# Kernel optimization log

Hardware: AMD Instinct MI355X
Metric: run time of the kernel (lower is better)

The kernel has to match this reference:

```python
import jax, jax.numpy as jnp
import numpy as np

B, N, DIM, H = 4, 16384, 384, 8
C = DIM // H          # head_dim = 48
M = C // 2            # kernel_ratio=0.5 -> m = 24
EPS = 1e-6

def setup_inputs() -> dict:
    key = jax.random.key(0)
    k0, k1, k2, k3, k4 = jax.random.split(key, 5)
    x = jax.random.normal(k0, (B, N, DIM), jnp.float32)
    # small init scale keeps exp() in the kernel feature map well-conditioned
    qkv_w = jax.random.normal(k1, (3 * DIM, DIM), jnp.float32) * 0.02
    proj_w = jax.random.normal(k2, (DIM, DIM), jnp.float32) * 0.02
    proj_b = jax.random.normal(k3, (DIM,), jnp.float32) * 0.02
    # per-head orthogonal random features (rows orthonormal), scaled by sqrt(m)
    g = jax.random.normal(k4, (H, C, M), jnp.float32)
    q_mat, _ = jnp.linalg.qr(g)                  # (H, C, M), orthonormal columns
    w = jnp.transpose(q_mat, (0, 2, 1)) * np.sqrt(M)  # (H, M, C)
    return {"x": x, "qkv_w": qkv_w, "proj_w": proj_w, "proj_b": proj_b, "w": w}

def _feature_map(t, w, scale):
    # t: [B,H,N,C], w: [H,M,C]
    t = t * scale
    logits = jnp.einsum('bhnc,hmc->bhnm', t, w) - 0.5 * jnp.sum(t * t, axis=-1, keepdims=True)
    return jnp.exp(logits) / np.sqrt(w.shape[1])

def reference(x, qkv_w, proj_w, proj_b, w):
    b, n, dim = x.shape
    h, m, c = w.shape
    scale = c ** (-0.25)
    # qkv projection, split into q,k,v with layout (qkv H C)
    qkv = (x @ qkv_w.T).reshape(b, n, 3, h, c).transpose(2, 0, 3, 1, 4)  # [3,B,H,N,C]
    q, k, v = qkv[0], qkv[1], qkv[2]
    phi_q = _feature_map(q, w, scale)   # [B,H,N,M]
    phi_k = _feature_map(k, w, scale)   # [B,H,N,M]
    # normalizer: q . sum_n(k)
    D = jnp.einsum('bhnm,bhm->bhn', phi_q, phi_k.sum(axis=2)) + EPS  # [B,H,N]
    # linear-attention state: K^T V, then Q @ (K^T V)
    ktv = jnp.einsum('bhnm,bhnc->bhmc', phi_k, v)                    # [B,H,M,C]
    out = jnp.einsum('bhnm,bhmc->bhnc', phi_q, ktv) / D[..., None]   # [B,H,N,C]
    out = out.transpose(0, 2, 1, 3).reshape(b, n, dim)               # [B,N,dim]
    return out @ proj_w.T + proj_b
```

## Files before the change

kernel.cpp:

```cpp
#include <hip/hip_runtime.h>
#include <hip/hip_bf16.h>

typedef __bf16 bf16x8 __attribute__((ext_vector_type(8)));
typedef float  f32x4  __attribute__((ext_vector_type(4)));
typedef short  short8 __attribute__((ext_vector_type(8)));
typedef float  f32x4v __attribute__((ext_vector_type(4)));

#define B_SZ 4
#define N_SZ 16384
#define DIM_SZ 384
#define H_SZ 8
#define C_SZ 48
#define M_SZ 24

static constexpr float SCALE = 0.37991784282579627f;
static constexpr float RSM   = 0.20412414523193154f;
static constexpr float EPS_V = 1e-6f;


__device__ __forceinline__ void gld_lds16(void* lds, const void* g) {
  __builtin_amdgcn_global_load_lds(
      (const __attribute__((address_space(1))) unsigned int*)g,
      (__attribute__((address_space(3))) unsigned int*)lds, 16, 0, 0);
}

__device__ __forceinline__ float bf2f(short s) {
  union { unsigned u; float f; } cv;
  cv.u = ((unsigned)(unsigned short)s) << 16;
  return cv.f;
}
__device__ __forceinline__ short f2bf_s(float f) {
  const __bf16 b = (__bf16)f;
  return __builtin_bit_cast(short, b);
}

template<int EPI>
__global__ __launch_bounds__(256, 2) void gemm2b(
    const __bf16* __restrict__ A, const __bf16* __restrict__ Bm,
    void* __restrict__ Cout, const float* __restrict__ bias,
    int M, int Nw, int K,
    size_t aSlice, size_t bSlice, size_t cSlice) {
  extern __shared__ __align__(16) char lds[];
  const int t    = threadIdx.x;
  const int lane = t & 63;
  const int wid  = t >> 6;
  const int wm   = wid >> 1;
  const int wn   = wid & 1;
  const int l15  = lane & 15;
  const int kgq  = lane >> 4;

  const int bz = blockIdx.z;
  const __bf16* Ab = A  + (size_t)bz * aSlice;
  const __bf16* Bb = Bm + (size_t)bz * bSlice;

  const int gx   = gridDim.x;
  const int nwg  = gx * gridDim.y;
  const int orig = blockIdx.y * gx + blockIdx.x;
  const int qq   = nwg >> 3, rr = nwg & 7;
  const int xcd  = orig & 7, pos = orig >> 3;
  const int id   = (xcd < rr ? xcd*(qq+1) : rr*(qq+1) + (xcd-rr)*qq) + pos;
  const int row0 = (id / gx) * 128, col0 = (id % gx) * 128;

  const int nt = K >> 6;

  const int sg = (t & 7) ^ ((t >> 3) & 7);

  auto stage = [&](int kt) {
    char* buf = lds + (kt & 1) * 32768;
    const size_t kofs = (size_t)kt * 64 + sg * 8;
    #pragma unroll
    for (int i = 0; i < 4; ++i) {
      const int r = i*32 + (t >> 3);
      gld_lds16(buf + i*4096 + t*16,         Ab + (size_t)(row0 + r) * K + kofs);
      gld_lds16(buf + 16384 + i*4096 + t*16, Bb + (size_t)(col0 + r) * K + kofs);
    }
  };

  f32x4 acc[4][4] = {};

  stage(0);

  for (int kt = 0; kt < nt; ++kt) {
    asm volatile("s_waitcnt vmcnt(0)" ::: "memory");
    __builtin_amdgcn_s_barrier();
    __builtin_amdgcn_sched_barrier(0);

    char* buf = lds + (kt & 1) * 32768;
    if (kt + 1 < nt) stage(kt + 1);

    bf16x8 bfr[4][2];
    #pragma unroll
    for (int ni = 0; ni < 4; ++ni) {
      const int brow = wn*64 + ni*16 + l15;
      #pragma unroll
      for (int kk = 0; kk < 2; ++kk)
        bfr[ni][kk] = *(const bf16x8*)(buf + 16384 + brow*128
                          + ((kk*64 + kgq*16) ^ ((brow & 7) << 4)));
    }
    #pragma unroll
    for (int mi = 0; mi < 4; ++mi) {
      const int arow = wm*64 + mi*16 + l15;
      const bf16x8 a0 = *(const bf16x8*)(buf + arow*128
                          + ((kgq*16)      ^ ((arow & 7) << 4)));
      const bf16x8 a1 = *(const bf16x8*)(buf + arow*128
                          + ((64 + kgq*16) ^ ((arow & 7) << 4)));
      __builtin_amdgcn_s_setprio(1);
      #pragma unroll
      for (int ni = 0; ni < 4; ++ni) {
        acc[mi][ni] = __builtin_amdgcn_mfma_f32_16x16x32_bf16(a0, bfr[ni][0], acc[mi][ni], 0,0,0);
        acc[mi][ni] = __builtin_amdgcn_mfma_f32_16x16x32_bf16(a1, bfr[ni][1], acc[mi][ni], 0,0,0);
      }
      __builtin_amdgcn_s_setprio(0);
    }
  }

  const int cr = (lane >> 4) << 2;
  #pragma unroll
  for (int mi = 0; mi < 4; ++mi) {
    #pragma unroll
    for (int ni = 0; ni < 4; ++ni) {
      const int col = col0 + wn*64 + ni*16 + l15;
      #pragma unroll
      for (int j = 0; j < 4; ++j) {
        const int row = row0 + wm*64 + mi*16 + cr + j;
        const float v = acc[mi][ni][j];
        if (EPI == 1) {
          ((float*)Cout + (size_t)bz*cSlice)[(size_t)row * Nw + col] = v + bias[col];
        } else {
          ((__bf16*)Cout + (size_t)bz*cSlice)[(size_t)row * Nw + col] = (__bf16)v;
        }
      }
    }
  }
}

__global__ __launch_bounds__(256) void wlog_kernel(
    const float* __restrict__ qkv_w, const float* __restrict__ w,
    __bf16* __restrict__ Baug) {
  const int idx = blockIdx.x * 256 + threadIdx.x;
  if (idx >= 2*192*384) return;
  const int d = idx % 384, rs = idx / 384;
  const int side = rs / 192, hm = rs % 192;
  const int h = hm / 24;
  const float* wr = w + (size_t)hm * 48;
  const float* qw = qkv_w + ((size_t)(side*384 + h*48)) * 384 + d;
  float acc = 0.f;
  #pragma unroll
  for (int c = 0; c < 48; ++c)
    acc += wr[c] * qw[(size_t)c * 384];
  Baug[(size_t)(768 + side*192 + hm) * 384 + d] = (__bf16)(acc * SCALE);
}

__global__ __launch_bounds__(256) void ktv_fused(
    const __bf16* __restrict__ kvll, float* __restrict__ ktv_f,
    float* __restrict__ ksum) {
  const int b = blockIdx.z, h = blockIdx.y, sp = blockIdx.x;
  const int t = threadIdx.x, wv = t >> 6, lane = t & 63;
  const int l15 = lane & 15, g = lane >> 4;
  const int bh = b*H_SZ + h;
  __shared__ __align__(16) __bf16 vT[4][48][40];
  __shared__ __align__(16) __bf16 phiT[4][24][40];
  __shared__ float red[4][1152];
  f32x4 acc[2][3] = {};
  f32x4 aks[2] = {};
  const int nbase = sp*512 + wv*128;

  bf16x8 ones{};
  if (l15 == 0)
    #pragma unroll
    for (int j = 0; j < 8; ++j) ones[j] = (__bf16)1.0f;

  for (int step = 0; step < 4; ++step) {
    const int n0 = nbase + step*32;
    #pragma unroll
    for (int it = 0; it < 3; ++it) {
      const int task = it*64 + lane;
      const int tk = task / 6, p = task % 6;
      const short8 r = *(const short8*)(kvll + ((size_t)(b*N_SZ) + n0 + tk)*1152
                                            + 384 + h*C_SZ + p*8);
      #pragma unroll
      for (int e = 0; e < 8; ++e)
        vT[wv][p*8 + e][tk] = __builtin_bit_cast(__bf16, (short)r[e]);
    }
    if (lane < 32) {
      const __bf16* row = kvll + ((size_t)(b*N_SZ) + n0 + lane)*1152 + h*C_SZ;
      float ss = 0.f;
      #pragma unroll
      for (int i = 0; i < 6; ++i) {
        const short8 r = *(const short8*)(row + i*8);
        #pragma unroll
        for (int j = 0; j < 8; ++j) { const float f = bf2f(r[j]) * SCALE; ss += f*f; }
      }
      const float hs = 0.5f * ss;
      const __bf16* lk = kvll + ((size_t)(b*N_SZ) + n0 + lane)*1152 + 960 + h*24;
      #pragma unroll
      for (int i = 0; i < 3; ++i) {
        const short8 r = *(const short8*)(lk + i*8);
        #pragma unroll
        for (int j = 0; j < 8; ++j)
          phiT[wv][i*8 + j][lane] = (__bf16)(__expf(bf2f(r[j]) - hs) * RSM);
      }
    }
    const bf16x8 a0 = *(const bf16x8*)(&phiT[wv][l15][g*8]);
    bf16x8 a1{};
    if (l15 < 8) a1 = *(const bf16x8*)(&phiT[wv][16 + l15][g*8]);
    #pragma unroll
    for (int ct = 0; ct < 3; ++ct) {
      const bf16x8 bfr = *(const bf16x8*)(&vT[wv][ct*16 + l15][g*8]);
      acc[0][ct] = __builtin_amdgcn_mfma_f32_16x16x32_bf16(a0, bfr, acc[0][ct], 0,0,0);
      acc[1][ct] = __builtin_amdgcn_mfma_f32_16x16x32_bf16(a1, bfr, acc[1][ct], 0,0,0);
    }
    aks[0] = __builtin_amdgcn_mfma_f32_16x16x32_bf16(a0, ones, aks[0], 0,0,0);
    aks[1] = __builtin_amdgcn_mfma_f32_16x16x32_bf16(a1, ones, aks[1], 0,0,0);
  }

  if (l15 == 0) {
    #pragma unroll
    for (int mt = 0; mt < 2; ++mt)
      #pragma unroll
      for (int jj = 0; jj < 4; ++jj) {
        const int m = mt*16 + g*4 + jj;
        if (m < 24) atomicAdd(&ksum[bh*24 + m], aks[mt][jj]);
      }
  }
  #pragma unroll
  for (int mt = 0; mt < 2; ++mt)
    #pragma unroll
    for (int ct = 0; ct < 3; ++ct)
      #pragma unroll
      for (int jj = 0; jj < 4; ++jj) {
        const int row = mt*16 + g*4 + jj;
        if (row < 24)
          red[wv][row*48 + ct*16 + l15] = acc[mt][ct][jj];
      }
  __syncthreads();
  for (int i = t; i < 1152; i += 256) {
    const float s = red[0][i] + red[1][i] + red[2][i] + red[3][i];
    atomicAdd(&ktv_f[bh*1152 + i], s);
  }
}

__global__ __launch_bounds__(256) void gt_kernel(
    const float* __restrict__ ktv_f, const float* __restrict__ proj_w,
    __bf16* __restrict__ Gt) {
  const int idx = blockIdx.x * 256 + threadIdx.x;
  if (idx >= 4*384*192) return;
  const int hm = idx % 192, o = (idx / 192) % 384, b = idx / (192*384);
  const int h = hm / 24, m = hm % 24;
  const float* kt = ktv_f + ((size_t)(b*H_SZ + h))*1152 + m*48;
  const float* pw = proj_w + (size_t)o*384 + h*48;
  float acc = 0.f;
  #pragma unroll
  for (int c = 0; c < 48; ++c) acc += kt[c] * pw[c];
  Gt[((size_t)b*384 + o)*192 + hm] = (__bf16)acc;
}

__global__ __launch_bounds__(256) void pprime_kernel(
    const __bf16* __restrict__ kvll, const float* __restrict__ ksum,
    __bf16* __restrict__ Pp) {
  const int tok = blockIdx.x * 256 + threadIdx.x;
  const int b = (blockIdx.x * 256) >> 14;
  __shared__ float ksl[192];
  if (threadIdx.x < 192) ksl[threadIdx.x] = ksum[b*192 + threadIdx.x];
  __syncthreads();

  const __bf16* lq = kvll + (size_t)tok*1152 + 768;
  __bf16* po = Pp + (size_t)tok*192;
  #pragma unroll
  for (int h = 0; h < 8; ++h) {
    float ph[24];
    float d = EPS_V;
    #pragma unroll
    for (int i = 0; i < 3; ++i) {
      const short8 r = *(const short8*)(lq + h*24 + i*8);
      #pragma unroll
      for (int j = 0; j < 8; ++j) {
        const float p = __expf(bf2f(r[j])) * RSM;
        ph[i*8 + j] = p;
        d += p * ksl[h*24 + i*8 + j];
      }
    }
    const float inv = 1.0f / d;
    #pragma unroll
    for (int i = 0; i < 3; ++i) {
      short8 pk;
      #pragma unroll
      for (int j = 0; j < 8; ++j) pk[j] = f2bf_s(ph[i*8 + j] * inv);
      *(short8*)(po + h*24 + i*8) = pk;
    }
  }
}

__global__ __launch_bounds__(256) void f32_to_bf16_kernel(
    const float* __restrict__ in, __bf16* __restrict__ out, int n8) {
  const int i = blockIdx.x * blockDim.x + threadIdx.x;
  if (i >= n8) return;
  const f32x4v a = *(const f32x4v*)(in + (size_t)i*8);
  const f32x4v c = *(const f32x4v*)(in + (size_t)i*8 + 4);
  short8 pk;
  #pragma unroll
  for (int j = 0; j < 4; ++j) {
    pk[j]     = f2bf_s(a[j]);
    pk[4 + j] = f2bf_s(c[j]);
  }
  *(short8*)(out + (size_t)i*8) = pk;
}

extern "C" void kernel_launch(void* const* d_in, const int* in_sizes, int n_in,
                              void* d_out, int out_size, void* d_ws, size_t ws_size,
                              hipStream_t stream) {
  (void)in_sizes; (void)n_in; (void)out_size; (void)ws_size;
  const float* x      = (const float*)d_in[0];
  const float* qkv_w  = (const float*)d_in[1];
  const float* proj_w = (const float*)d_in[2];
  const float* proj_b = (const float*)d_in[3];
  const float* w      = (const float*)d_in[4];
  float* out = (float*)d_out;

  const size_t BN_TOT = (size_t)B_SZ * N_SZ;
  char* ws = (char*)d_ws;
  size_t off = 0;
  auto alloc = [&](size_t bytes) {
    char* p = ws + off;
    off += (bytes + 255) & ~(size_t)255;
    return p;
  };
  __bf16* x_bf  = (__bf16*)alloc(BN_TOT * DIM_SZ * 2);
  __bf16* Baug  = (__bf16*)alloc((size_t)1152 * 384 * 2);
  __bf16* kvll  = (__bf16*)alloc(BN_TOT * 1152 * 2);
  float*  ktv_f = (float*)alloc((size_t)32 * 1152 * 4);
  float*  ksum  = (float*)alloc((size_t)32 * 24 * 4);
  __bf16* Pp    = (__bf16*)alloc(BN_TOT * 192 * 2);
  __bf16* Gt    = (__bf16*)alloc((size_t)B_SZ * 384 * 192 * 2);

  hipMemsetAsync(ktv_f, 0, (size_t)32 * 1152 * 4, stream);
  hipMemsetAsync(ksum,  0, (size_t)32 * 24 * 4, stream);

  static const int LDS_BYTES = 2 * 32768;
  hipFuncSetAttribute(reinterpret_cast<const void*>(&gemm2b<0>),
                      hipFuncAttributeMaxDynamicSharedMemorySize, LDS_BYTES);
  hipFuncSetAttribute(reinterpret_cast<const void*>(&gemm2b<1>),
                      hipFuncAttributeMaxDynamicSharedMemorySize, LDS_BYTES);

  {
    const int n8x = (int)(BN_TOT * DIM_SZ / 8);
    f32_to_bf16_kernel<<<(n8x + 255)/256, 256, 0, stream>>>(x, x_bf, n8x);
    const int n8kv = 768 * 384 / 8;
    f32_to_bf16_kernel<<<(n8kv + 255)/256, 256, 0, stream>>>(
        qkv_w + (size_t)384 * 384, Baug, n8kv);
    wlog_kernel<<<(2*192*384 + 255)/256, 256, 0, stream>>>(qkv_w, w, Baug);
  }

  gemm2b<0><<<dim3(1152/128, BN_TOT/128, 1), 256, LDS_BYTES, stream>>>(
      x_bf, Baug, kvll, nullptr, (int)BN_TOT, 1152, DIM_SZ, 0, 0, 0);

  ktv_fused<<<dim3(32, H_SZ, B_SZ), 256, 0, stream>>>(kvll, ktv_f, ksum);

  gt_kernel<<<(4*384*192 + 255)/256, 256, 0, stream>>>(ktv_f, proj_w, Gt);
  pprime_kernel<<<(int)(BN_TOT/256), 256, 0, stream>>>(kvll, ksum, Pp);

  gemm2b<1><<<dim3(384/128, N_SZ/128, B_SZ), 256, LDS_BYTES, stream>>>(
      Pp, Gt, out, proj_b, N_SZ, 384, 192,
      (size_t)N_SZ * 192, (size_t)384 * 192, (size_t)N_SZ * 384);
}
```

Before: 229.3 us.

## Replace QKV GEMM with 256x256-tile 8-wave ping-pong pipelined kernel

```diff
diff --git a/kernel.cpp b/kernel.cpp
--- a/kernel.cpp
+++ b/kernel.cpp
@@ -32,6 +32,149 @@
 __device__ __forceinline__ short f2bf_s(float f) {
   const __bf16 b = (__bf16)f;
   return __builtin_bit_cast(short, b);
+}
+__device__ __forceinline__ f32x4 MF(bf16x8 a, bf16x8 b, f32x4 c) {
+  return __builtin_amdgcn_mfma_f32_16x16x32_bf16(a, b, c, 0, 0, 0);
+}
+__device__ __forceinline__ void bar_lgkm() {
+  __builtin_amdgcn_s_barrier();
+  asm volatile("s_waitcnt lgkmcnt(0)" ::: "memory");
+  __builtin_amdgcn_sched_barrier(0);
+}
+__device__ __forceinline__ void bar2() {
+  __builtin_amdgcn_s_barrier();
+  __builtin_amdgcn_sched_barrier(0);
+}
+__device__ __forceinline__ void mfmaq(f32x4 (&ac)[4][2],
+                                      const bf16x8 (&a)[4][2],
+                                      const bf16x8 (&b)[2][2]) {
+  __builtin_amdgcn_s_setprio(1);
+  #pragma unroll
+  for (int mf = 0; mf < 4; ++mf) {
+    ac[mf][0] = MF(a[mf][0], b[0][0], ac[mf][0]);
+    ac[mf][0] = MF(a[mf][1], b[0][1], ac[mf][0]);
+    ac[mf][1] = MF(a[mf][0], b[1][0], ac[mf][1]);
+    ac[mf][1] = MF(a[mf][1], b[1][1], ac[mf][1]);
+  }
+  __builtin_amdgcn_s_setprio(0);
+}
+
+__global__ __launch_bounds__(512, 2) void gemm8p(
+    const __bf16* __restrict__ A, const __bf16* __restrict__ Bm,
+    __bf16* __restrict__ Cout, int Nw, int K) {
+  extern __shared__ __align__(16) char lds[];
+  const int t    = threadIdx.x;
+  const int lane = t & 63;
+  const int wid  = t >> 6;
+  const int wm   = wid >> 2;
+  const int wn   = wid & 3;
+  const int l15  = lane & 15;
+  const int kgq  = lane >> 4;
+
+  const int gx   = gridDim.x;
+  const int nwg  = gx * gridDim.y;
+  const int orig = blockIdx.y * gx + blockIdx.x;
+  const int qq   = nwg >> 3, rr = nwg & 7;
+  const int xcd  = orig & 7, pos = orig >> 3;
+  const int id   = (xcd < rr ? xcd*(qq+1) : rr*(qq+1) + (xcd-rr)*qq) + pos;
+  const int row0 = (id / gx) * 256, col0 = (id % gx) * 256;
+
+  const int nt = K >> 6;
+  const int sg = (t & 7) ^ ((t >> 3) & 7);
+
+  auto stageh = [&](int k, int isB, int half) {
+    if (k >= nt) return;
+    char* base = lds + (k & 1) * 65536 + isB * 32768;
+    const __bf16* src = isB ? (Bm + (size_t)col0 * K) : (A + (size_t)row0 * K);
+    #pragma unroll
+    for (int i = 0; i < 2; ++i) {
+      const int r = half*128 + i*64 + (t >> 3);
+      gld_lds16(base + r*128 + (t & 7)*16,
+                src + (size_t)r * K + (size_t)k*64 + sg*8);
+    }
+  };
+  auto loadA = [&](const char* buf, int qm, bf16x8 (&af)[4][2]) {
+    #pragma unroll
+    for (int mf = 0; mf < 4; ++mf) {
+      const int r = qm*128 + wm*64 + mf*16 + l15;
+      af[mf][0] = *(const bf16x8*)(buf + r*128 + ((kgq*16)      ^ ((r&7)<<4)));
+      af[mf][1] = *(const bf16x8*)(buf + r*128 + ((64 + kgq*16) ^ ((r&7)<<4)));
+    }
+  };
+  auto loadB = [&](const char* buf, int qn, bf16x8 (&bq)[2][2]) {
+    #pragma unroll
+    for (int nf = 0; nf < 2; ++nf) {
+      const int r = qn*128 + wn*32 + nf*16 + l15;
+      bq[nf][0] = *(const bf16x8*)(buf + 32768 + r*128 + ((kgq*16)      ^ ((r&7)<<4)));
+      bq[nf][1] = *(const bf16x8*)(buf + 32768 + r*128 + ((64 + kgq*16) ^ ((r&7)<<4)));
+    }
+  };
+
+  f32x4 acc[2][2][4][2] = {};
+  bf16x8 af[4][2], bq0[2][2], bq1[2][2];
+
+  stageh(0, 0, 0); stageh(0, 1, 0); stageh(0, 0, 1); stageh(0, 1, 1);
+  stageh(1, 0, 0); stageh(1, 1, 0);
+  asm volatile("s_waitcnt vmcnt(4)" ::: "memory");
+  __builtin_amdgcn_s_barrier();
+  __builtin_amdgcn_sched_barrier(0);
+
+  const int nIter = nt >> 1;
+  for (int it = 0; it < nIter; ++it) {
+    const int kt1 = 2*it + 1, kt2 = 2*it + 2, kt3 = 2*it + 3;
+    char* b0 = lds;
+    char* b1 = lds + 65536;
+    const bool lastIt = (it == nIter - 1);
+
+    loadA(b0, 0, af); loadB(b0, 0, bq0);
+    stageh(kt1, 0, 1);
+    bar_lgkm(); mfmaq(acc[0][0], af, bq0); bar2();
+    loadB(b0, 1, bq1);
+    stageh(kt1, 1, 1);
+    bar_lgkm(); mfmaq(acc[0][1], af, bq1); bar2();
+    loadA(b0, 1, af);
+    stageh(kt2, 0, 0);
+    bar_lgkm(); mfmaq(acc[1][0], af, bq0); bar2();
+    stageh(kt2, 1, 0);
+    if (lastIt) asm volatile("s_waitcnt vmcnt(0)" ::: "memory");
+    else        asm volatile("s_waitcnt vmcnt(4)" ::: "memory");
+    __builtin_amdgcn_s_barrier();
+    __builtin_amdgcn_sched_barrier(0);
+    mfmaq(acc[1][1], af, bq1); bar2();
+    loadA(b1, 0, af); loadB(b1, 0, bq0);
+    stageh(kt2, 0, 1);
+    bar_lgkm(); mfmaq(acc[0][0], af, bq0); bar2();
+    loadB(b1, 1, bq1);
+    stageh(kt2, 1, 1);
+    bar_lgkm(); mfmaq(acc[0][1], af, bq1); bar2();
+    loadA(b1, 1, af);
+    stageh(kt3, 0, 0);
+    bar_lgkm(); mfmaq(acc[1][0], af, bq0); bar2();
+    stageh(kt3, 1, 0);
+    if (!lastIt) asm volatile("s_waitcnt vmcnt(4)" ::: "memory");
+    __builtin_amdgcn_s_barrier();
+    __builtin_amdgcn_sched_barrier(0);
+    mfmaq(acc[1][1], af, bq1); bar2();
+  }
+
+  const int cr = (lane >> 4) << 2;
+  #pragma unroll
+  for (int qm = 0; qm < 2; ++qm)
+    #pragma unroll
+    for (int qn = 0; qn < 2; ++qn)
+      #pragma unroll
+      for (int mf = 0; mf < 4; ++mf)
+        #pragma unroll
+        for (int nf = 0; nf < 2; ++nf) {
+          const int col = col0 + qn*128 + wn*32 + nf*16 + l15;
+          if (col < Nw) {
+            #pragma unroll
+            for (int j = 0; j < 4; ++j) {
+              const int row = row0 + qm*128 + wm*64 + mf*16 + cr + j;
+              Cout[(size_t)row * Nw + col] = (__bf16)acc[qm][qn][mf][nf][j];
+            }
+          }
+        }
 }
 
 template<int EPI>
@@ -62,7 +205,6 @@
   const int row0 = (id / gx) * 128, col0 = (id % gx) * 128;
 
   const int nt = K >> 6;
-
   const int sg = (t & 7) ^ ((t >> 3) & 7);
 
   auto stage = [&](int kt) {
@@ -77,7 +219,6 @@
   };
 
   f32x4 acc[4][4] = {};
-
   stage(0);
 
   for (int kt = 0; kt < nt; ++kt) {
@@ -107,8 +248,8 @@
       __builtin_amdgcn_s_setprio(1);
       #pragma unroll
       for (int ni = 0; ni < 4; ++ni) {
-        acc[mi][ni] = __builtin_amdgcn_mfma_f32_16x16x32_bf16(a0, bfr[ni][0], acc[mi][ni], 0,0,0);
-        acc[mi][ni] = __builtin_amdgcn_mfma_f32_16x16x32_bf16(a1, bfr[ni][1], acc[mi][ni], 0,0,0);
+        acc[mi][ni] = MF(a0, bfr[ni][0], acc[mi][ni]);
+        acc[mi][ni] = MF(a1, bfr[ni][1], acc[mi][ni]);
       }
       __builtin_amdgcn_s_setprio(0);
     }
@@ -207,11 +348,11 @@
     #pragma unroll
     for (int ct = 0; ct < 3; ++ct) {
       const bf16x8 bfr = *(const bf16x8*)(&vT[wv][ct*16 + l15][g*8]);
-      acc[0][ct] = __builtin_amdgcn_mfma_f32_16x16x32_bf16(a0, bfr, acc[0][ct], 0,0,0);
-      acc[1][ct] = __builtin_amdgcn_mfma_f32_16x16x32_bf16(a1, bfr, acc[1][ct], 0,0,0);
-    }
-    aks[0] = __builtin_amdgcn_mfma_f32_16x16x32_bf16(a0, ones, aks[0], 0,0,0);
-    aks[1] = __builtin_amdgcn_mfma_f32_16x16x32_bf16(a1, ones, aks[1], 0,0,0);
+      acc[0][ct] = MF(a0, bfr, acc[0][ct]);
+      acc[1][ct] = MF(a1, bfr, acc[1][ct]);
+    }
+    aks[0] = MF(a0, ones, aks[0]);
+    aks[1] = MF(a1, ones, aks[1]);
   }
 
   if (l15 == 0) {
@@ -326,7 +467,7 @@
     return p;
   };
   __bf16* x_bf  = (__bf16*)alloc(BN_TOT * DIM_SZ * 2);
-  __bf16* Baug  = (__bf16*)alloc((size_t)1152 * 384 * 2);
+  __bf16* Baug  = (__bf16*)alloc((size_t)1280 * 384 * 2);
   __bf16* kvll  = (__bf16*)alloc(BN_TOT * 1152 * 2);
   float*  ktv_f = (float*)alloc((size_t)32 * 1152 * 4);
   float*  ksum  = (float*)alloc((size_t)32 * 24 * 4);
@@ -336,11 +477,12 @@
   hipMemsetAsync(ktv_f, 0, (size_t)32 * 1152 * 4, stream);
   hipMemsetAsync(ksum,  0, (size_t)32 * 24 * 4, stream);
 
-  static const int LDS_BYTES = 2 * 32768;
-  hipFuncSetAttribute(reinterpret_cast<const void*>(&gemm2b<0>),
-                      hipFuncAttributeMaxDynamicSharedMemorySize, LDS_BYTES);
+  static const int LDS8P = 2 * 65536;
+  static const int LDS2B = 2 * 32768;
+  hipFuncSetAttribute(reinterpret_cast<const void*>(&gemm8p),
+                      hipFuncAttributeMaxDynamicSharedMemorySize, LDS8P);
   hipFuncSetAttribute(reinterpret_cast<const void*>(&gemm2b<1>),
-                      hipFuncAttributeMaxDynamicSharedMemorySize, LDS_BYTES);
+                      hipFuncAttributeMaxDynamicSharedMemorySize, LDS2B);
 
   {
     const int n8x = (int)(BN_TOT * DIM_SZ / 8);
@@ -351,15 +493,15 @@
     wlog_kernel<<<(2*192*384 + 255)/256, 256, 0, stream>>>(qkv_w, w, Baug);
   }
 
-  gemm2b<0><<<dim3(1152/128, BN_TOT/128, 1), 256, LDS_BYTES, stream>>>(
-      x_bf, Baug, kvll, nullptr, (int)BN_TOT, 1152, DIM_SZ, 0, 0, 0);
+  gemm8p<<<dim3(1280/256, BN_TOT/256), 512, LDS8P, stream>>>(
+      x_bf, Baug, kvll, 1152, DIM_SZ);
 
   ktv_fused<<<dim3(32, H_SZ, B_SZ), 256, 0, stream>>>(kvll, ktv_f, ksum);
 
   gt_kernel<<<(4*384*192 + 255)/256, 256, 0, stream>>>(ktv_f, proj_w, Gt);
   pprime_kernel<<<(int)(BN_TOT/256), 256, 0, stream>>>(kvll, ksum, Pp);
 
-  gemm2b<1><<<dim3(384/128, N_SZ/128, B_SZ), 256, LDS_BYTES, stream>>>(
+  gemm2b<1><<<dim3(384/128, N_SZ/128, B_SZ), 256, LDS2B, stream>>>(
       Pp, Gt, out, proj_b, N_SZ, 384, 192,
       (size_t)N_SZ * 192, (size_t)384 * 192, (size_t)N_SZ * 384);
 }
```

After: 255.5 us. 1.11x slower.

## Add single-buffered BK=128 QKV GEMM and double ktv_fused grid split

Applied to the files above, without the earlier changes.

```diff
diff --git a/kernel.cpp b/kernel.cpp
--- a/kernel.cpp
+++ b/kernel.cpp
@@ -32,6 +32,105 @@
 __device__ __forceinline__ short f2bf_s(float f) {
   const __bf16 b = (__bf16)f;
   return __builtin_bit_cast(short, b);
+}
+__device__ __forceinline__ f32x4 MF(bf16x8 a, bf16x8 b, f32x4 c) {
+  return __builtin_amdgcn_mfma_f32_16x16x32_bf16(a, b, c, 0, 0, 0);
+}
+
+__global__ __launch_bounds__(256, 2) void gemm1k(
+    const __bf16* __restrict__ A, const __bf16* __restrict__ Bm,
+    __bf16* __restrict__ Cout, int Nw, int K) {
+  extern __shared__ __align__(16) char lds[];
+  const int t    = threadIdx.x;
+  const int lane = t & 63;
+  const int wid  = t >> 6;
+  const int wm   = wid >> 1;
+  const int wn   = wid & 1;
+  const int l15  = lane & 15;
+  const int kgq  = lane >> 4;
+
+  const int gx   = gridDim.x;
+  const int nwg  = gx * gridDim.y;
+  const int orig = blockIdx.y * gx + blockIdx.x;
+  const int qq   = nwg >> 3, rr = nwg & 7;
+  const int xcd  = orig & 7, pos = orig >> 3;
+  const int id   = (xcd < rr ? xcd*(qq+1) : rr*(qq+1) + (xcd-rr)*qq) + pos;
+  const int row0 = (id / gx) * 128, col0 = (id % gx) * 128;
+
+  const int nt = K >> 7;
+
+  const int sg = ((t & 15) ^ ((t >> 4) & 7)) * 8;
+
+  auto stage = [&](int kt) {
+    const size_t kofs = (size_t)kt * 128 + sg;
+    #pragma unroll
+    for (int i = 0; i < 8; ++i) {
+      const int r = i*16 + (t >> 4);
+      gld_lds16(lds + r*256 + (t & 15)*16,
+                A + (size_t)(row0 + r) * K + kofs);
+      gld_lds16(lds + 32768 + r*256 + (t & 15)*16,
+                Bm + (size_t)(col0 + r) * K + kofs);
+    }
+  };
+
+  f32x4 acc[4][4] = {};
+  stage(0);
+  asm volatile("s_waitcnt vmcnt(0)" ::: "memory");
+  __builtin_amdgcn_s_barrier();
+  __builtin_amdgcn_sched_barrier(0);
+
+  for (int kt = 0; kt < nt; ++kt) {
+    bf16x8 af[4][4], bfr[4][4];
+    #pragma unroll
+    for (int mi = 0; mi < 4; ++mi) {
+      const int a = wm*64 + mi*16 + l15;
+      #pragma unroll
+      for (int kk = 0; kk < 4; ++kk)
+        af[mi][kk] = *(const bf16x8*)(lds + a*256
+                        + ((kk*64 + kgq*16) ^ ((a & 7) << 4)));
+    }
+    #pragma unroll
+    for (int ni = 0; ni < 4; ++ni) {
+      const int b = wn*64 + ni*16 + l15;
+      #pragma unroll
+      for (int kk = 0; kk < 4; ++kk)
+        bfr[ni][kk] = *(const bf16x8*)(lds + 32768 + b*256
+                        + ((kk*64 + kgq*16) ^ ((b & 7) << 4)));
+    }
+    asm volatile("s_waitcnt lgkmcnt(0)" ::: "memory");
+    __builtin_amdgcn_sched_barrier(0);
+    __builtin_amdgcn_s_barrier();
+    __builtin_amdgcn_sched_barrier(0);
+    if (kt + 1 < nt) stage(kt + 1);
+    __builtin_amdgcn_s_setprio(1);
+    #pragma unroll
+    for (int kk = 0; kk < 4; ++kk)
+      #pragma unroll
+      for (int mi = 0; mi < 4; ++mi)
+        #pragma unroll
+        for (int ni = 0; ni < 4; ++ni)
+          acc[mi][ni] = MF(af[mi][kk], bfr[ni][kk], acc[mi][ni]);
+    __builtin_amdgcn_s_setprio(0);
+    if (kt + 1 < nt) {
+      asm volatile("s_waitcnt vmcnt(0)" ::: "memory");
+      __builtin_amdgcn_s_barrier();
+      __builtin_amdgcn_sched_barrier(0);
+    }
+  }
+
+  const int cr = (lane >> 4) << 2;
+  #pragma unroll
+  for (int mi = 0; mi < 4; ++mi) {
+    #pragma unroll
+    for (int ni = 0; ni < 4; ++ni) {
+      const int col = col0 + wn*64 + ni*16 + l15;
+      #pragma unroll
+      for (int j = 0; j < 4; ++j) {
+        const int row = row0 + wm*64 + mi*16 + cr + j;
+        Cout[(size_t)row * Nw + col] = (__bf16)acc[mi][ni][j];
+      }
+    }
+  }
 }
 
 template<int EPI>
@@ -62,7 +161,6 @@
   const int row0 = (id / gx) * 128, col0 = (id % gx) * 128;
 
   const int nt = K >> 6;
-
   const int sg = (t & 7) ^ ((t >> 3) & 7);
 
   auto stage = [&](int kt) {
@@ -77,7 +175,6 @@
   };
 
   f32x4 acc[4][4] = {};
-
   stage(0);
 
   for (int kt = 0; kt < nt; ++kt) {
@@ -107,8 +204,8 @@
       __builtin_amdgcn_s_setprio(1);
       #pragma unroll
       for (int ni = 0; ni < 4; ++ni) {
-        acc[mi][ni] = __builtin_amdgcn_mfma_f32_16x16x32_bf16(a0, bfr[ni][0], acc[mi][ni], 0,0,0);
-        acc[mi][ni] = __builtin_amdgcn_mfma_f32_16x16x32_bf16(a1, bfr[ni][1], acc[mi][ni], 0,0,0);
+        acc[mi][ni] = MF(a0, bfr[ni][0], acc[mi][ni]);
+        acc[mi][ni] = MF(a1, bfr[ni][1], acc[mi][ni]);
       }
       __builtin_amdgcn_s_setprio(0);
     }
@@ -163,14 +260,14 @@
   __shared__ float red[4][1152];
   f32x4 acc[2][3] = {};
   f32x4 aks[2] = {};
-  const int nbase = sp*512 + wv*128;
+  const int nbase = sp*256 + wv*64;
 
   bf16x8 ones{};
   if (l15 == 0)
     #pragma unroll
     for (int j = 0; j < 8; ++j) ones[j] = (__bf16)1.0f;
 
-  for (int step = 0; step < 4; ++step) {
+  for (int step = 0; step < 2; ++step) {
     const int n0 = nbase + step*32;
     #pragma unroll
     for (int it = 0; it < 3; ++it) {
@@ -207,11 +304,11 @@
     #pragma unroll
     for (int ct = 0; ct < 3; ++ct) {
       const bf16x8 bfr = *(const bf16x8*)(&vT[wv][ct*16 + l15][g*8]);
-      acc[0][ct] = __builtin_amdgcn_mfma_f32_16x16x32_bf16(a0, bfr, acc[0][ct], 0,0,0);
-      acc[1][ct] = __builtin_amdgcn_mfma_f32_16x16x32_bf16(a1, bfr, acc[1][ct], 0,0,0);
-    }
-    aks[0] = __builtin_amdgcn_mfma_f32_16x16x32_bf16(a0, ones, aks[0], 0,0,0);
-    aks[1] = __builtin_amdgcn_mfma_f32_16x16x32_bf16(a1, ones, aks[1], 0,0,0);
+      acc[0][ct] = MF(a0, bfr, acc[0][ct]);
+      acc[1][ct] = MF(a1, bfr, acc[1][ct]);
+    }
+    aks[0] = MF(a0, ones, aks[0]);
+    aks[1] = MF(a1, ones, aks[1]);
   }
 
   if (l15 == 0) {
@@ -336,11 +433,12 @@
   hipMemsetAsync(ktv_f, 0, (size_t)32 * 1152 * 4, stream);
   hipMemsetAsync(ksum,  0, (size_t)32 * 24 * 4, stream);
 
-  static const int LDS_BYTES = 2 * 32768;
-  hipFuncSetAttribute(reinterpret_cast<const void*>(&gemm2b<0>),
-                      hipFuncAttributeMaxDynamicSharedMemorySize, LDS_BYTES);
+  static const int LDS1K = 65536;
+  static const int LDS2B = 2 * 32768;
+  hipFuncSetAttribute(reinterpret_cast<const void*>(&gemm1k),
+                      hipFuncAttributeMaxDynamicSharedMemorySize, LDS1K);
   hipFuncSetAttribute(reinterpret_cast<const void*>(&gemm2b<1>),
-                      hipFuncAttributeMaxDynamicSharedMemorySize, LDS_BYTES);
+                      hipFuncAttributeMaxDynamicSharedMemorySize, LDS2B);
 
   {
     const int n8x = (int)(BN_TOT * DIM_SZ / 8);
@@ -351,15 +449,15 @@
     wlog_kernel<<<(2*192*384 + 255)/256, 256, 0, stream>>>(qkv_w, w, Baug);
   }
 
-  gemm2b<0><<<dim3(1152/128, BN_TOT/128, 1), 256, LDS_BYTES, stream>>>(
-      x_bf, Baug, kvll, nullptr, (int)BN_TOT, 1152, DIM_SZ, 0, 0, 0);
-
-  ktv_fused<<<dim3(32, H_SZ, B_SZ), 256, 0, stream>>>(kvll, ktv_f, ksum);
+  gemm1k<<<dim3(1152/128, BN_TOT/128), 256, LDS1K, stream>>>(
+      x_bf, Baug, kvll, 1152, DIM_SZ);
+
+  ktv_fused<<<dim3(64, H_SZ, B_SZ), 256, 0, stream>>>(kvll, ktv_f, ksum);
 
   gt_kernel<<<(4*384*192 + 255)/256, 256, 0, stream>>>(ktv_f, proj_w, Gt);
   pprime_kernel<<<(int)(BN_TOT/256), 256, 0, stream>>>(kvll, ksum, Pp);
 
-  gemm2b<1><<<dim3(384/128, N_SZ/128, B_SZ), 256, LDS_BYTES, stream>>>(
+  gemm2b<1><<<dim3(384/128, N_SZ/128, B_SZ), 256, LDS2B, stream>>>(
       Pp, Gt, out, proj_b, N_SZ, 384, 192,
       (size_t)N_SZ * 192, (size_t)384 * 192, (size_t)N_SZ * 384);
 }
```

New measurement: 281.5 us. +22.8%, slower.

## Replace atomic ktv accumulation with per-block partials and a separate reduce kernel

Applied to the files above, without the earlier changes.

```diff
diff --git a/kernel.cpp b/kernel.cpp
--- a/kernel.cpp
+++ b/kernel.cpp
@@ -32,6 +32,9 @@
 __device__ __forceinline__ short f2bf_s(float f) {
   const __bf16 b = (__bf16)f;
   return __builtin_bit_cast(short, b);
+}
+__device__ __forceinline__ f32x4 MF(bf16x8 a, bf16x8 b, f32x4 c) {
+  return __builtin_amdgcn_mfma_f32_16x16x32_bf16(a, b, c, 0, 0, 0);
 }
 
 template<int EPI>
@@ -62,7 +65,6 @@
   const int row0 = (id / gx) * 128, col0 = (id % gx) * 128;
 
   const int nt = K >> 6;
-
   const int sg = (t & 7) ^ ((t >> 3) & 7);
 
   auto stage = [&](int kt) {
@@ -77,7 +79,6 @@
   };
 
   f32x4 acc[4][4] = {};
-
   stage(0);
 
   for (int kt = 0; kt < nt; ++kt) {
@@ -107,8 +108,8 @@
       __builtin_amdgcn_s_setprio(1);
       #pragma unroll
       for (int ni = 0; ni < 4; ++ni) {
-        acc[mi][ni] = __builtin_amdgcn_mfma_f32_16x16x32_bf16(a0, bfr[ni][0], acc[mi][ni], 0,0,0);
-        acc[mi][ni] = __builtin_amdgcn_mfma_f32_16x16x32_bf16(a1, bfr[ni][1], acc[mi][ni], 0,0,0);
+        acc[mi][ni] = MF(a0, bfr[ni][0], acc[mi][ni]);
+        acc[mi][ni] = MF(a1, bfr[ni][1], acc[mi][ni]);
       }
       __builtin_amdgcn_s_setprio(0);
     }
@@ -152,25 +153,24 @@
 }
 
 __global__ __launch_bounds__(256) void ktv_fused(
-    const __bf16* __restrict__ kvll, float* __restrict__ ktv_f,
-    float* __restrict__ ksum) {
+    const __bf16* __restrict__ kvll, float* __restrict__ ktv_part) {
   const int b = blockIdx.z, h = blockIdx.y, sp = blockIdx.x;
   const int t = threadIdx.x, wv = t >> 6, lane = t & 63;
   const int l15 = lane & 15, g = lane >> 4;
   const int bh = b*H_SZ + h;
   __shared__ __align__(16) __bf16 vT[4][48][40];
   __shared__ __align__(16) __bf16 phiT[4][24][40];
-  __shared__ float red[4][1152];
+  __shared__ float red[4][1184];
   f32x4 acc[2][3] = {};
   f32x4 aks[2] = {};
-  const int nbase = sp*512 + wv*128;
+  const int nbase = sp*256 + wv*64;
 
   bf16x8 ones{};
   if (l15 == 0)
     #pragma unroll
     for (int j = 0; j < 8; ++j) ones[j] = (__bf16)1.0f;
 
-  for (int step = 0; step < 4; ++step) {
+  for (int step = 0; step < 2; ++step) {
     const int n0 = nbase + step*32;
     #pragma unroll
     for (int it = 0; it < 3; ++it) {
@@ -207,22 +207,13 @@
     #pragma unroll
     for (int ct = 0; ct < 3; ++ct) {
       const bf16x8 bfr = *(const bf16x8*)(&vT[wv][ct*16 + l15][g*8]);
-      acc[0][ct] = __builtin_amdgcn_mfma_f32_16x16x32_bf16(a0, bfr, acc[0][ct], 0,0,0);
-      acc[1][ct] = __builtin_amdgcn_mfma_f32_16x16x32_bf16(a1, bfr, acc[1][ct], 0,0,0);
-    }
-    aks[0] = __builtin_amdgcn_mfma_f32_16x16x32_bf16(a0, ones, aks[0], 0,0,0);
-    aks[1] = __builtin_amdgcn_mfma_f32_16x16x32_bf16(a1, ones, aks[1], 0,0,0);
-  }
-
-  if (l15 == 0) {
-    #pragma unroll
-    for (int mt = 0; mt < 2; ++mt)
-      #pragma unroll
-      for (int jj = 0; jj < 4; ++jj) {
-        const int m = mt*16 + g*4 + jj;
-        if (m < 24) atomicAdd(&ksum[bh*24 + m], aks[mt][jj]);
-      }
-  }
+      acc[0][ct] = MF(a0, bfr, acc[0][ct]);
+      acc[1][ct] = MF(a1, bfr, acc[1][ct]);
+    }
+    aks[0] = MF(a0, ones, aks[0]);
+    aks[1] = MF(a1, ones, aks[1]);
+  }
+
   #pragma unroll
   for (int mt = 0; mt < 2; ++mt)
     #pragma unroll
@@ -233,10 +224,34 @@
         if (row < 24)
           red[wv][row*48 + ct*16 + l15] = acc[mt][ct][jj];
       }
+  if (l15 == 0) {
+    #pragma unroll
+    for (int mt = 0; mt < 2; ++mt)
+      #pragma unroll
+      for (int jj = 0; jj < 4; ++jj) {
+        const int m = mt*16 + g*4 + jj;
+        if (m < 24) red[wv][1152 + m] = aks[mt][jj];
+      }
+  }
   __syncthreads();
-  for (int i = t; i < 1152; i += 256) {
-    const float s = red[0][i] + red[1][i] + red[2][i] + red[3][i];
-    atomicAdd(&ktv_f[bh*1152 + i], s);
+  float* outp = ktv_part + ((size_t)bh*64 + sp) * 1184;
+  for (int i = t; i < 1176; i += 256)
+    outp[i] = red[0][i] + red[1][i] + red[2][i] + red[3][i];
+}
+
+__global__ __launch_bounds__(256) void reduce_ktv(
+    const float* __restrict__ ktv_part, float* __restrict__ ktv_f,
+    float* __restrict__ ksum) {
+  const int bh = blockIdx.x >> 2, q = blockIdx.x & 3;
+  const int i0 = q * 296;
+  const int iend = (i0 + 296 < 1176) ? i0 + 296 : 1176;
+  for (int i = i0 + threadIdx.x; i < iend; i += 256) {
+    float s = 0.f;
+    #pragma unroll 8
+    for (int sp = 0; sp < 64; ++sp)
+      s += ktv_part[((size_t)bh*64 + sp) * 1184 + i];
+    if (i < 1152) ktv_f[bh*1152 + i] = s;
+    else          ksum[bh*24 + (i - 1152)] = s;
   }
 }
 
@@ -325,22 +340,20 @@
     off += (bytes + 255) & ~(size_t)255;
     return p;
   };
-  __bf16* x_bf  = (__bf16*)alloc(BN_TOT * DIM_SZ * 2);
-  __bf16* Baug  = (__bf16*)alloc((size_t)1152 * 384 * 2);
-  __bf16* kvll  = (__bf16*)alloc(BN_TOT * 1152 * 2);
-  float*  ktv_f = (float*)alloc((size_t)32 * 1152 * 4);
-  float*  ksum  = (float*)alloc((size_t)32 * 24 * 4);
-  __bf16* Pp    = (__bf16*)alloc(BN_TOT * 192 * 2);
-  __bf16* Gt    = (__bf16*)alloc((size_t)B_SZ * 384 * 192 * 2);
-
-  hipMemsetAsync(ktv_f, 0, (size_t)32 * 1152 * 4, stream);
-  hipMemsetAsync(ksum,  0, (size_t)32 * 24 * 4, stream);
-
-  static const int LDS_BYTES = 2 * 32768;
+  __bf16* x_bf     = (__bf16*)alloc(BN_TOT * DIM_SZ * 2);
+  __bf16* Baug     = (__bf16*)alloc((size_t)1152 * 384 * 2);
+  __bf16* kvll     = (__bf16*)alloc(BN_TOT * 1152 * 2);
+  float*  ktv_part = (float*)alloc((size_t)32 * 64 * 1184 * 4);
+  float*  ktv_f    = (float*)alloc((size_t)32 * 1152 * 4);
+  float*  ksum     = (float*)alloc((size_t)32 * 24 * 4);
+  __bf16* Pp       = (__bf16*)alloc(BN_TOT * 192 * 2);
+  __bf16* Gt       = (__bf16*)alloc((size_t)B_SZ * 384 * 192 * 2);
+
+  static const int LDS2B = 2 * 32768;
   hipFuncSetAttribute(reinterpret_cast<const void*>(&gemm2b<0>),
-                      hipFuncAttributeMaxDynamicSharedMemorySize, LDS_BYTES);
+                      hipFuncAttributeMaxDynamicSharedMemorySize, LDS2B);
   hipFuncSetAttribute(reinterpret_cast<const void*>(&gemm2b<1>),
-                      hipFuncAttributeMaxDynamicSharedMemorySize, LDS_BYTES);
+                      hipFuncAttributeMaxDynamicSharedMemorySize, LDS2B);
 
   {
     const int n8x = (int)(BN_TOT * DIM_SZ / 8);
@@ -351,15 +364,16 @@
     wlog_kernel<<<(2*192*384 + 255)/256, 256, 0, stream>>>(qkv_w, w, Baug);
   }
 
-  gemm2b<0><<<dim3(1152/128, BN_TOT/128, 1), 256, LDS_BYTES, stream>>>(
+  gemm2b<0><<<dim3(1152/128, BN_TOT/128, 1), 256, LDS2B, stream>>>(
       x_bf, Baug, kvll, nullptr, (int)BN_TOT, 1152, DIM_SZ, 0, 0, 0);
 
-  ktv_fused<<<dim3(32, H_SZ, B_SZ), 256, 0, stream>>>(kvll, ktv_f, ksum);
+  ktv_fused<<<dim3(64, H_SZ, B_SZ), 256, 0, stream>>>(kvll, ktv_part);
+  reduce_ktv<<<128, 256, 0, stream>>>(ktv_part, ktv_f, ksum);
 
   gt_kernel<<<(4*384*192 + 255)/256, 256, 0, stream>>>(ktv_f, proj_w, Gt);
   pprime_kernel<<<(int)(BN_TOT/256), 256, 0, stream>>>(kvll, ksum, Pp);
 
-  gemm2b<1><<<dim3(384/128, N_SZ/128, B_SZ), 256, LDS_BYTES, stream>>>(
+  gemm2b<1><<<dim3(384/128, N_SZ/128, B_SZ), 256, LDS2B, stream>>>(
       Pp, Gt, out, proj_b, N_SZ, 384, 192,
       (size_t)N_SZ * 192, (size_t)384 * 192, (size_t)N_SZ * 384);
 }
```

After: 196.6 us. 14.3% less time.
